# Kernel optimization log

Measured on AMD Instinct MI355X. Metric: run time of the kernel, lower is better.

The kernel has to match this reference:

```python
import jax, jax.numpy as jnp
import numpy as np
import math

IN_FEATURES = 4096
OUT_FEATURES = 4096
NUM_COMPONENTS = 256
TWO_PI = 2.0 * math.pi


def setup_inputs() -> dict:
    key = jax.random.key(0)
    k1, k2, k3, k4 = jax.random.split(key, 4)
    x = jax.random.normal(k1, (4096, IN_FEATURES), dtype=jnp.float32)
    mus = jax.random.uniform(k2, (NUM_COMPONENTS, 2), dtype=jnp.float32)
    log_vars = -3.0 - jax.random.uniform(k3, (NUM_COMPONENTS, 2), dtype=jnp.float32)
    weights = jax.random.uniform(k4, (NUM_COMPONENTS,), dtype=jnp.float32) / NUM_COMPONENTS
    return {"x": x, "mus": mus, "log_vars": log_vars, "weights": weights}


def reference(x, mus, log_vars, weights):
    in_features = x.shape[1]
    x_in_idx = jnp.linspace(0.0, 1.0, in_features, dtype=jnp.float32)    # [I]
    x_out_idx = jnp.linspace(0.0, 1.0, OUT_FEATURES, dtype=jnp.float32)  # [O]
    vars_ = jnp.exp(log_vars)  # [M, 2]

    # Input-side Gaussian basis, fused with 1/sqrt(2*pi*var) and component weight: [I, M]
    d_in = (x_in_idx[:, None] - mus[None, :, 0]) ** 2
    G_in = jnp.exp(-d_in / (2.0 * vars_[None, :, 0])) / jnp.sqrt(TWO_PI * vars_[None, :, 0]) * weights[None, :]
    C = x @ G_in  # [B, M]

    # Output-side Gaussian pdf (Normal(mu1, sigma1).log_prob(x_out).exp()): [M, O]
    d_out = (x_out_idx[None, :] - mus[:, 1:2]) ** 2
    G_out = jnp.exp(-d_out / (2.0 * vars_[:, 1:2])) / jnp.sqrt(TWO_PI * vars_[:, 1:2])

    x_out = (C @ G_out) / (in_features * jnp.sum(weights))  # [B, O]
    return x_out
```

## Files before the change

kernel.cpp:

```cpp
#include <hip/hip_runtime.h>
#include <hip/hip_bf16.h>
#include <math.h>

#define IN_FEAT 4096
#define OUT_FEAT 4096
#define NCOMP 256
#define BATCH 4096
#define TWO_PI_F 6.28318530717958647692f

typedef __attribute__((ext_vector_type(8))) short short8;
typedef __attribute__((ext_vector_type(8))) __bf16 bf16x8;
typedef __attribute__((ext_vector_type(4))) float f32x4;
typedef __attribute__((ext_vector_type(16))) float f32x16;

__device__ __forceinline__ ushort f2b(float f) {
  union { float f; unsigned u; } v; v.f = f;
  unsigned r = (v.u + 0x7fffu + ((v.u >> 16) & 1u)) >> 16;
  return (ushort)r;
}

__device__ __forceinline__ float b2f(short s) {
  union { unsigned u; float f; } v; v.u = ((unsigned)(ushort)s) << 16;
  return v.f;
}

__device__ __forceinline__ bf16x8 ld_frag(const void* p) {
  short8 s = *(const short8*)p;
  return __builtin_bit_cast(bf16x8, s);
}

__device__ __forceinline__ ushort4 cvt4s(float4 a) {
  ushort4 h;
  h.x = f2b(a.x); h.y = f2b(a.y); h.z = f2b(a.z); h.w = f2b(a.w);
  return h;
}

__device__ __forceinline__ void gload_lds16(const void* g, void* l) {
  __builtin_amdgcn_global_load_lds(
      (const __attribute__((address_space(1))) void*)g,
      (__attribute__((address_space(3))) void*)l, 16, 0, 0);
}

__global__ __launch_bounds__(256) void prep_kernel(
    const float* __restrict__ mus, const float* __restrict__ lvs,
    const float* __restrict__ w,
    ushort* __restrict__ Gt, ushort* __restrict__ GoT) {
  int idx = blockIdx.x * 256 + threadIdx.x;
  if (idx < NCOMP * IN_FEAT) {
    int m = idx >> 12, i = idx & (IN_FEAT - 1);
    float v = expf(lvs[2 * m]);
    float d = (float)i * (1.0f / (IN_FEAT - 1)) - mus[2 * m];
    float g = expf(-d * d * (0.5f / v)) * rsqrtf(TWO_PI_F * v) * w[m];
    Gt[idx] = f2b(g);
  } else {
    idx -= NCOMP * IN_FEAT;
    int o = idx >> 8, m = idx & (NCOMP - 1);
    float v = expf(lvs[2 * m + 1]);
    float d = (float)o * (1.0f / (OUT_FEAT - 1)) - mus[2 * m + 1];
    float g = expf(-d * d * (0.5f / v)) * rsqrtf(TWO_PI_F * v);
    GoT[idx] = f2b(g);
  }
}

template<int NS>
__global__ __launch_bounds__(512, 2) void gemm1_kernel(
    const float* __restrict__ x, const ushort* __restrict__ Gt,
    ushort* __restrict__ Cpart) {
  constexpr int KR = IN_FEAT / NS;
  constexpr int NCH = KR / 64;
  __shared__ __align__(16) ushort Bs[2 * 16384];
  __shared__ __align__(16) ushort xs[2 * 4096];
  const int tid = threadIdx.x, wid = tid >> 6, lane = tid & 63;
  const int l15 = lane & 15, q = lane >> 4;
  const int rg = wid >> 1, h2 = wid & 1;
  const int m0 = blockIdx.x * 64;
  const int kb0 = blockIdx.y * KR;

  const int brow = lane >> 2;
  const int bsw = (((lane & 3) ^ ((lane >> 3) & 3)) << 3);
  const int fswz = (q << 4) ^ (((l15 >> 1) & 3) << 4);

  const int xrow = tid >> 4, xslot = tid & 15;
  const float* xsrc0 = &x[(size_t)(m0 + xrow) * IN_FEAT + kb0 + xslot * 4];
  const float* xsrc1 = xsrc0 + (size_t)32 * IN_FEAT;
  const int wb0 = xrow * 128 + ((((xslot >> 1) ^ (xrow & 7)) << 4) | ((xslot & 1) << 3));
  const int wb1 = (xrow + 32) * 128 +
                  ((((xslot >> 1) ^ ((xrow + 32) & 7)) << 4) | ((xslot & 1) << 3));

  const int arow = rg * 16 + l15;
  const int akey = arow & 7;

  f32x4 acc[8] = {};
  float4 Pa0, Pa1, Pb0, Pb1;

  #define STAGE_B(buf, kc)                                                   \
    _Pragma("unroll")                                                        \
    for (int i_ = 0; i_ < 4; ++i_) {                                         \
      int idx_ = wid * 4 + i_, seg_ = idx_ >> 4, nf_ = idx_ & 15;            \
      gload_lds16(&Gt[(size_t)(nf_ * 16 + brow) * IN_FEAT + kb0 +            \
                      (kc) * 64 + seg_ * 32 + bsw],                          \
                  &Bs[(buf) * 16384 + seg_ * 8192 + nf_ * 512]);             \
    }

  #define LOAD_W(P0, P1, wn)                                                 \
    P0 = *(const float4*)(xsrc0 + (wn) * 64);                                \
    P1 = *(const float4*)(xsrc1 + (wn) * 64);

  #define WRITE_W(P0, P1, buf) {                                             \
    char* xb_ = (char*)xs + (buf) * 8192;                                    \
    *(ushort4*)(xb_ + wb0) = cvt4s(P0);                                      \
    *(ushort4*)(xb_ + wb1) = cvt4s(P1);                                      \
  }

  #define COMPUTE(kc) {                                                      \
    const char* Xb = (const char*)xs + ((kc) & 1) * 8192;                    \
    const char* Bb = (const char*)Bs + ((kc) & 1) * 32768;                   \
    _Pragma("unroll")                                                        \
    for (int st = 0; st < 2; ++st) {                                         \
      bf16x8 a = ld_frag(Xb + arow * 128 + (((st * 4 + q) ^ akey) << 4));    \
      const char* sb = Bb + st * 16384;                                      \
      _Pragma("unroll")                                                      \
      for (int j = 0; j < 8; ++j) {                                          \
        bf16x8 b = ld_frag(sb + ((h2 * 8 + j) * 16 + l15) * 64 + fswz);      \
        acc[j] = __builtin_amdgcn_mfma_f32_16x16x32_bf16(a, b, acc[j], 0, 0, 0); \
      }                                                                      \
    } }

  STAGE_B(0, 0)
  LOAD_W(Pa0, Pa1, 0)
  LOAD_W(Pb0, Pb1, 1)
  asm volatile("s_waitcnt vmcnt(2)" ::: "memory");
  __builtin_amdgcn_sched_barrier(0);
  WRITE_W(Pa0, Pa1, 0)
  asm volatile("s_waitcnt lgkmcnt(0)" ::: "memory");
  __builtin_amdgcn_s_barrier();
  __builtin_amdgcn_sched_barrier(0);

  #pragma unroll
  for (int kc = 0; kc < NCH; ++kc) {
    if (kc < NCH - 1) {
      STAGE_B((kc + 1) & 1, kc + 1)
      int wn = (kc + 2 < NCH) ? (kc + 2) : (NCH - 1);
      if ((kc & 1) == 0) { LOAD_W(Pa0, Pa1, wn) }
      else              { LOAD_W(Pb0, Pb1, wn) }
    }
    COMPUTE(kc)
    if (kc < NCH - 1) {
      asm volatile("s_waitcnt vmcnt(6)" ::: "memory");
      __builtin_amdgcn_sched_barrier(0);
      if ((kc & 1) == 0) { WRITE_W(Pb0, Pb1, 1) }
      else              { WRITE_W(Pa0, Pa1, 0) }
      asm volatile("s_waitcnt vmcnt(2) lgkmcnt(0)" ::: "memory");
      __builtin_amdgcn_s_barrier();
      __builtin_amdgcn_sched_barrier(0);
    }
  }
  #undef STAGE_B
  #undef LOAD_W
  #undef WRITE_W
  #undef COMPUTE

  ushort* Cp = Cpart + (size_t)blockIdx.y * ((size_t)BATCH * NCOMP);
  #pragma unroll
  for (int j = 0; j < 8; ++j)
    #pragma unroll
    for (int r = 0; r < 4; ++r) {
      int row = m0 + rg * 16 + q * 4 + r;
      int col = h2 * 128 + j * 16 + l15;
      Cp[(size_t)row * NCOMP + col] = f2b(acc[j][r]);
    }
}

template<int NS>
__global__ __launch_bounds__(256) void reduce_kernel(ushort* __restrict__ Cp) {
  size_t i = ((size_t)blockIdx.x * 256 + threadIdx.x) * 8;
  float s[8] = {};
  #pragma unroll
  for (int p = 0; p < NS; ++p) {
    short8 v = *(const short8*)&Cp[(size_t)p * BATCH * NCOMP + i];
    #pragma unroll
    for (int e = 0; e < 8; ++e) s[e] += b2f(v[e]);
  }
  short8 hh;
  #pragma unroll
  for (int e = 0; e < 8; ++e) hh[e] = (short)f2b(s[e]);
  *(short8*)&Cp[i] = hh;
}

__global__ __launch_bounds__(256, 4) void gemm2_kernel(
    const ushort* __restrict__ Cb, const ushort* __restrict__ GoT,
    const float* __restrict__ w, float* __restrict__ out) {
  __shared__ __align__(16) ushort lds[2 * 8192];
  const int tid = threadIdx.x, wid = tid >> 6, lane = tid & 63;
  const int m0 = blockIdx.y * 128, n0 = blockIdx.x * 128;
  const int wr = (wid >> 1) * 64, wc = (wid & 1) * 64;
  const int r32 = lane & 31, h = lane >> 5;

  float4 wv = *(const float4*)&w[lane * 4];
  float s = wv.x + wv.y + wv.z + wv.w;
  #pragma unroll
  for (int off = 32; off > 0; off >>= 1) s += __shfl_xor(s, off);
  const float scale = 1.0f / ((float)IN_FEAT * s);

  const int brow = lane >> 2;
  const int bswz = (((lane & 3) ^ ((lane >> 3) & 3)) << 3);
  const int sw0 = (h << 4) ^ (((r32 >> 1) & 3) << 4);

  f32x16 acc[2][2] = {};

  #define STAGE2(buf, k0)                                                    \
    _Pragma("unroll")                                                        \
    for (int q2 = 0; q2 < 2; ++q2) {                                         \
      int c = wid * 2 + q2;                                                  \
      int row = c * 16 + brow;                                               \
      gload_lds16(&Cb[(size_t)(m0 + row) * NCOMP + (k0) + bswz],             \
                  &lds[(buf) * 8192 + c * 512]);                             \
      gload_lds16(&GoT[(size_t)(n0 + row) * NCOMP + (k0) + bswz],            \
                  &lds[(buf) * 8192 + 4096 + c * 512]);                      \
    }

  STAGE2(0, 0)
  __syncthreads();

  for (int t = 0; t < 8; ++t) {
    if (t < 7) STAGE2((t + 1) & 1, (t + 1) * 32)
    const char* base = (const char*)lds + (t & 1) * 16384;
    const char* Bb = base + 8192;
    #pragma unroll
    for (int s2 = 0; s2 < 2; ++s2) {
      const int off = sw0 ^ (s2 << 5);
      bf16x8 a0 = ld_frag(base + (wr + r32) * 64 + off);
      bf16x8 a1 = ld_frag(base + (wr + 32 + r32) * 64 + off);
      bf16x8 b0 = ld_frag(Bb + (wc + r32) * 64 + off);
      bf16x8 b1 = ld_frag(Bb + (wc + 32 + r32) * 64 + off);
      acc[0][0] = __builtin_amdgcn_mfma_f32_32x32x16_bf16(a0, b0, acc[0][0], 0, 0, 0);
      acc[0][1] = __builtin_amdgcn_mfma_f32_32x32x16_bf16(a0, b1, acc[0][1], 0, 0, 0);
      acc[1][0] = __builtin_amdgcn_mfma_f32_32x32x16_bf16(a1, b0, acc[1][0], 0, 0, 0);
      acc[1][1] = __builtin_amdgcn_mfma_f32_32x32x16_bf16(a1, b1, acc[1][1], 0, 0, 0);
    }
    __syncthreads();
  }
  #undef STAGE2

  #pragma unroll
  for (int mi = 0; mi < 2; ++mi)
    #pragma unroll
    for (int nj = 0; nj < 2; ++nj)
      #pragma unroll
      for (int g = 0; g < 16; ++g) {
        int row = m0 + wr + mi * 32 + (g & 3) + 8 * (g >> 2) + 4 * h;
        int col = n0 + wc + nj * 32 + r32;
        out[(size_t)row * OUT_FEAT + col] = acc[mi][nj][g] * scale;
      }
}

extern "C" void kernel_launch(void* const* d_in, const int* in_sizes, int n_in,
                              void* d_out, int out_size, void* d_ws, size_t ws_size,
                              hipStream_t stream) {
  const float* x   = (const float*)d_in[0];
  const float* mus = (const float*)d_in[1];
  const float* lvs = (const float*)d_in[2];
  const float* w   = (const float*)d_in[3];
  float* out = (float*)d_out;

  ushort* Gt  = (ushort*)d_ws;
  ushort* GoT = Gt  + (size_t)NCOMP * IN_FEAT;
  ushort* Cpart = GoT + (size_t)OUT_FEAT * NCOMP;

  const size_t MiB = 1024 * 1024;
  int nsplit = 8;
  while (nsplit > 1 && ws_size < 4 * MiB + (size_t)nsplit * 2 * MiB + MiB)
    nsplit >>= 1;

  prep_kernel<<<(NCOMP * IN_FEAT + OUT_FEAT * NCOMP) / 256, 256, 0, stream>>>(
      mus, lvs, w, Gt, GoT);

  switch (nsplit) {
    case 8:
      gemm1_kernel<8><<<dim3(BATCH / 64, 8), 512, 0, stream>>>(x, Gt, Cpart);
      reduce_kernel<8><<<BATCH * NCOMP / 8 / 256, 256, 0, stream>>>(Cpart);
      break;
    case 4:
      gemm1_kernel<4><<<dim3(BATCH / 64, 4), 512, 0, stream>>>(x, Gt, Cpart);
      reduce_kernel<4><<<BATCH * NCOMP / 8 / 256, 256, 0, stream>>>(Cpart);
      break;
    case 2:
      gemm1_kernel<2><<<dim3(BATCH / 64, 2), 512, 0, stream>>>(x, Gt, Cpart);
      reduce_kernel<2><<<BATCH * NCOMP / 8 / 256, 256, 0, stream>>>(Cpart);
      break;
    default:
      gemm1_kernel<1><<<dim3(BATCH / 64, 1), 512, 0, stream>>>(x, Gt, Cpart);
      break;
  }

  gemm2_kernel<<<dim3(OUT_FEAT / 128, BATCH / 128), 256, 0, stream>>>(
      Cpart, GoT, w, out);
}
```

Baseline: 57.86 us.

## Restructure gemm1 pipeline with wide X staging and finer-grained B double buffering

The first GEMM now loads a 64x256 slab of x into shared memory once per window, where it used to load 64-column chunks. B (the Gaussian basis) is streamed in 32-wide K chunks with double buffering, and vmcnt waits are tuned so the next x window is prefetched in the middle of the current one. The aim is fewer x conversion/write phases and better overlap of global loads with MFMA work, at the cost of more barriers per K step and a different LDS footprint. The workspace threshold for choosing the split count is also relaxed, which may select a larger split factor.

Result: slower. 62.43 us (+7.9%).

```diff
diff --git a/kernel.cpp b/kernel.cpp
--- a/kernel.cpp
+++ b/kernel.cpp
@@ -67,9 +67,10 @@
     const float* __restrict__ x, const ushort* __restrict__ Gt,
     ushort* __restrict__ Cpart) {
   constexpr int KR = IN_FEAT / NS;
-  constexpr int NCH = KR / 64;
-  __shared__ __align__(16) ushort Bs[2 * 16384];
-  __shared__ __align__(16) ushort xs[2 * 4096];
+  constexpr int W = KR / 256;
+  constexpr int NCHT = KR / 32;
+  __shared__ __align__(16) ushort Bs[2 * 8192];
+  __shared__ __align__(16) ushort xs[64 * 256];
   const int tid = threadIdx.x, wid = tid >> 6, lane = tid & 63;
   const int l15 = lane & 15, q = lane >> 4;
   const int rg = wid >> 1, h2 = wid & 1;
@@ -80,85 +81,95 @@
   const int bsw = (((lane & 3) ^ ((lane >> 3) & 3)) << 3);
   const int fswz = (q << 4) ^ (((l15 >> 1) & 3) << 4);
 
-  const int xrow = tid >> 4, xslot = tid & 15;
-  const float* xsrc0 = &x[(size_t)(m0 + xrow) * IN_FEAT + kb0 + xslot * 4];
-  const float* xsrc1 = xsrc0 + (size_t)32 * IN_FEAT;
-  const int wb0 = xrow * 128 + ((((xslot >> 1) ^ (xrow & 7)) << 4) | ((xslot & 1) << 3));
-  const int wb1 = (xrow + 32) * 128 +
-                  ((((xslot >> 1) ^ ((xrow + 32) & 7)) << 4) | ((xslot & 1) << 3));
-
+  const float* xrow = &x[(size_t)(m0 + wid * 8) * IN_FEAT + kb0 + lane * 4];
   const int arow = rg * 16 + l15;
-  const int akey = arow & 7;
 
   f32x4 acc[8] = {};
-  float4 Pa0, Pa1, Pb0, Pb1;
-
-  #define STAGE_B(buf, kc)                                                   \
-    _Pragma("unroll")                                                        \
-    for (int i_ = 0; i_ < 4; ++i_) {                                         \
-      int idx_ = wid * 4 + i_, seg_ = idx_ >> 4, nf_ = idx_ & 15;            \
+  float4 X[8];
+
+  #define STAGE_B(buf, cg) {                                                 \
+    _Pragma("unroll")                                                        \
+    for (int i_ = 0; i_ < 2; ++i_) {                                         \
+      int nf_ = wid * 2 + i_;                                                \
       gload_lds16(&Gt[(size_t)(nf_ * 16 + brow) * IN_FEAT + kb0 +            \
-                      (kc) * 64 + seg_ * 32 + bsw],                          \
-                  &Bs[(buf) * 16384 + seg_ * 8192 + nf_ * 512]);             \
-    }
-
-  #define LOAD_W(P0, P1, wn)                                                 \
-    P0 = *(const float4*)(xsrc0 + (wn) * 64);                                \
-    P1 = *(const float4*)(xsrc1 + (wn) * 64);
-
-  #define WRITE_W(P0, P1, buf) {                                             \
-    char* xb_ = (char*)xs + (buf) * 8192;                                    \
-    *(ushort4*)(xb_ + wb0) = cvt4s(P0);                                      \
-    *(ushort4*)(xb_ + wb1) = cvt4s(P1);                                      \
-  }
-
-  #define COMPUTE(kc) {                                                      \
-    const char* Xb = (const char*)xs + ((kc) & 1) * 8192;                    \
-    const char* Bb = (const char*)Bs + ((kc) & 1) * 32768;                   \
-    _Pragma("unroll")                                                        \
-    for (int st = 0; st < 2; ++st) {                                         \
-      bf16x8 a = ld_frag(Xb + arow * 128 + (((st * 4 + q) ^ akey) << 4));    \
-      const char* sb = Bb + st * 16384;                                      \
-      _Pragma("unroll")                                                      \
-      for (int j = 0; j < 8; ++j) {                                          \
-        bf16x8 b = ld_frag(sb + ((h2 * 8 + j) * 16 + l15) * 64 + fswz);      \
-        acc[j] = __builtin_amdgcn_mfma_f32_16x16x32_bf16(a, b, acc[j], 0, 0, 0); \
-      }                                                                      \
+                      (cg) * 32 + bsw],                                      \
+                  &Bs[(buf) * 8192 + nf_ * 512]);                            \
     } }
 
+  #define ISSUE_X(wn) {                                                      \
+    _Pragma("unroll")                                                        \
+    for (int i_ = 0; i_ < 8; ++i_)                                           \
+      X[i_] = *(const float4*)(xrow + (size_t)i_ * IN_FEAT + (wn) * 256);    \
+    }
+
+  #define WRITE_X() {                                                        \
+    _Pragma("unroll")                                                        \
+    for (int i_ = 0; i_ < 8; ++i_) {                                         \
+      int r_ = wid * 8 + i_;                                                 \
+      int slot_ = (lane >> 1) ^ (r_ & 15);                                   \
+      *(ushort4*)((char*)xs + r_ * 512 + slot_ * 16 + (lane & 1) * 8) =      \
+          cvt4s(X[i_]);                                                      \
+    } }
+
+  #define WAITC(n)                                                           \
+    asm volatile("s_waitcnt vmcnt(" #n ")" ::: "memory");                    \
+    __builtin_amdgcn_s_barrier();                                            \
+    __builtin_amdgcn_sched_barrier(0);
+
+  #define COMPUTE(c) {                                                       \
+    bf16x8 a = ld_frag((const char*)xs + arow * 512 +                        \
+                       ((((c) * 4 + q) ^ l15) << 4));                        \
+    const char* bb = (const char*)Bs + ((c) & 1) * 16384;                    \
+    _Pragma("unroll")                                                        \
+    for (int j = 0; j < 8; ++j) {                                            \
+      bf16x8 b = ld_frag(bb + ((h2 * 8 + j) * 16 + l15) * 64 + fswz);        \
+      acc[j] = __builtin_amdgcn_mfma_f32_16x16x32_bf16(a, b, acc[j], 0, 0, 0); \
+    } }
+
+  #define ENDC(cg) {                                                         \
+    __builtin_amdgcn_s_barrier();                                            \
+    __builtin_amdgcn_sched_barrier(0);                                       \
+    if ((cg) + 2 < NCHT) STAGE_B(((cg) + 2) & 1, (cg) + 2)                   \
+    }
+
+  ISSUE_X(0)
   STAGE_B(0, 0)
-  LOAD_W(Pa0, Pa1, 0)
-  LOAD_W(Pb0, Pb1, 1)
-  asm volatile("s_waitcnt vmcnt(2)" ::: "memory");
+  STAGE_B(1, 1)
+  asm volatile("s_waitcnt vmcnt(4)" ::: "memory");
   __builtin_amdgcn_sched_barrier(0);
-  WRITE_W(Pa0, Pa1, 0)
+  WRITE_X()
   asm volatile("s_waitcnt lgkmcnt(0)" ::: "memory");
   __builtin_amdgcn_s_barrier();
   __builtin_amdgcn_sched_barrier(0);
 
-  #pragma unroll
-  for (int kc = 0; kc < NCH; ++kc) {
-    if (kc < NCH - 1) {
-      STAGE_B((kc + 1) & 1, kc + 1)
-      int wn = (kc + 2 < NCH) ? (kc + 2) : (NCH - 1);
-      if ((kc & 1) == 0) { LOAD_W(Pa0, Pa1, wn) }
-      else              { LOAD_W(Pb0, Pb1, wn) }
-    }
-    COMPUTE(kc)
-    if (kc < NCH - 1) {
-      asm volatile("s_waitcnt vmcnt(6)" ::: "memory");
-      __builtin_amdgcn_sched_barrier(0);
-      if ((kc & 1) == 0) { WRITE_W(Pb0, Pb1, 1) }
-      else              { WRITE_W(Pa0, Pa1, 0) }
-      asm volatile("s_waitcnt vmcnt(2) lgkmcnt(0)" ::: "memory");
+  for (int w = 0; w < W; ++w) {
+    const int base = w * 8;
+    const bool lastw = (w == W - 1);
+    if (w) {
+      WRITE_X()
+      asm volatile("s_waitcnt lgkmcnt(0)" ::: "memory");
       __builtin_amdgcn_s_barrier();
       __builtin_amdgcn_sched_barrier(0);
     }
+    WAITC(2) COMPUTE(0) ENDC(base + 0)
+    WAITC(2) COMPUTE(1) ENDC(base + 1)
+    if (!lastw) ISSUE_X(w + 1)
+    if (!lastw) { WAITC(10) } else { WAITC(2) }
+    COMPUTE(2) ENDC(base + 2)
+    if (!lastw) { WAITC(10) } else { WAITC(2) }
+    COMPUTE(3) ENDC(base + 3)
+    WAITC(2) COMPUTE(4) ENDC(base + 4)
+    WAITC(2) COMPUTE(5) ENDC(base + 5)
+    WAITC(2) COMPUTE(6) ENDC(base + 6)
+    if (!lastw) { WAITC(2) } else { WAITC(0) }
+    COMPUTE(7) ENDC(base + 7)
   }
   #undef STAGE_B
-  #undef LOAD_W
-  #undef WRITE_W
+  #undef ISSUE_X
+  #undef WRITE_X
+  #undef WAITC
   #undef COMPUTE
+  #undef ENDC
 
   ushort* Cp = Cpart + (size_t)blockIdx.y * ((size_t)BATCH * NCOMP);
   #pragma unroll
@@ -269,7 +280,7 @@
 
   const size_t MiB = 1024 * 1024;
   int nsplit = 8;
-  while (nsplit > 1 && ws_size < 4 * MiB + (size_t)nsplit * 2 * MiB + MiB)
+  while (nsplit > 1 && ws_size < 4 * MiB + (size_t)nsplit * 2 * MiB)
     nsplit >>= 1;
 
   prep_kernel<<<(NCOMP * IN_FEAT + OUT_FEAT * NCOMP) / 256, 256, 0, stream>>>(
```
